# Optimization experiments

Measured on AMD Instinct MI355X. Metric: run time of the kernel, lower is better.

The kernel has to match this reference:

```python
import jax, jax.numpy as jnp
import numpy as np

WS = 32          # window_size; N = WS*WS tokens
NH = 8           # num_heads
HD = 64          # head_dim
DIM = 512        # model dim (= NH*HD)
B = 16
N = WS * WS


def _rel_index() -> np.ndarray:
    """Relative position index, identical to the torch __init__ construction."""
    coords = np.stack(np.meshgrid(np.arange(WS), np.arange(WS), indexing='ij'))
    coords = coords.reshape(2, -1)                       # [2, N]
    rel = coords[:, :, None] - coords[:, None, :]        # [2, N, N]
    rel = rel.transpose(1, 2, 0).copy()                  # [N, N, 2]
    rel[..., 0] += WS - 1
    rel[..., 1] += WS - 1
    rel[..., 0] *= 2 * WS - 1
    return rel.sum(-1).astype(np.int32)                  # [N, N], values in [0, (2WS-1)^2)


def setup_inputs() -> dict:
    key = jax.random.key(0)
    ks = jax.random.split(key, 5)
    s = DIM ** -0.5
    return {
        "x": jax.random.normal(ks[0], (B, N, DIM), jnp.float32),
        "qkv_w": jax.random.normal(ks[1], (3 * NH * HD, DIM), jnp.float32) * s,
        "qkv_b": jnp.zeros((3 * NH * HD,), jnp.float32),
        "proj_w": jax.random.normal(ks[2], (DIM, NH * HD), jnp.float32) * s,
        "proj_b": jnp.zeros((DIM,), jnp.float32),
        "bias_table": jax.random.normal(ks[3], ((2 * WS - 1) ** 2, NH), jnp.float32) * 0.02,
        "rel_index": jnp.asarray(_rel_index()),
    }


def reference(x, qkv_w, qkv_b, proj_w, proj_b, bias_table, rel_index):
    Bb, Nn, C = x.shape
    qkv = (x @ qkv_w.T + qkv_b).reshape(Bb, Nn, 3, NH, HD)
    q, k, v = jnp.moveaxis(qkv, 2, 0)                    # each [B, N, NH, HD]
    q = q * (HD ** -0.5)
    attn = jnp.einsum('bnhd,bmhd->bhnm', q, k)           # [B, NH, N, N]
    bias = bias_table[rel_index]                         # gather -> [N, N, NH]
    attn = attn + jnp.transpose(bias, (2, 0, 1))[None]
    attn = jax.nn.softmax(attn, axis=-1)                 # dropout p=0 (eval)
    out = jnp.einsum('bhnm,bmhd->bnhd', attn, v).reshape(Bb, Nn, NH * HD)
    out = out @ proj_w.T + proj_b                        # [B, N, DIM]
    return jnp.transpose(out, (0, 2, 1)).reshape(Bb, DIM, WS, WS)
```

## Files before the change

kernel.cpp:

```cpp
#include <hip/hip_runtime.h>
#include <hip/hip_bf16.h>


typedef __attribute__((ext_vector_type(4))) float  f32x4;
typedef __attribute__((ext_vector_type(8))) short  s16x8;
typedef __attribute__((ext_vector_type(4))) short  s16x4;

#define LOG2E 1.44269504f

__device__ __forceinline__ short f2bf(float f) {
    union { float f; unsigned u; } v; v.f = f;
    unsigned r = v.u + 0x7fffu + ((v.u >> 16) & 1u);
    return (short)(r >> 16);
}
__device__ __forceinline__ float u2f(unsigned u) {
    union { unsigned u; float f; } v; v.u = u; return v.f;
}
__device__ __forceinline__ unsigned cvtpk(float lo, float hi) {
    unsigned r;
    asm("v_cvt_pk_bf16_f32 %0, %1, %2" : "=v"(r) : "v"(lo), "v"(hi));
    return r;
}
__device__ __forceinline__ s16x8 ld_frag(const short* p) {
    s16x4 lo = *(const s16x4*)p;
    s16x4 hi = *(const s16x4*)(p + 4);
    s16x8 v;
    v[0]=lo[0]; v[1]=lo[1]; v[2]=lo[2]; v[3]=lo[3];
    v[4]=hi[0]; v[5]=hi[1]; v[6]=hi[2]; v[7]=hi[3];
    return v;
}
__device__ __forceinline__ void st8(short* p, s16x8 v) {
    s16x4 lo, hi;
    lo[0]=v[0]; lo[1]=v[1]; lo[2]=v[2]; lo[3]=v[3];
    hi[0]=v[4]; hi[1]=v[5]; hi[2]=v[6]; hi[3]=v[7];
    *(s16x4*)p = lo;
    *(s16x4*)(p + 4) = hi;
}
__device__ __forceinline__ void gl_lds16(const short* g, short* l) {
    __builtin_amdgcn_global_load_lds(
        (const __attribute__((address_space(1))) unsigned int*)g,
        (__attribute__((address_space(3))) unsigned int*)l,
        16, 0, 0);
}

__global__ void cvt_kernel(const float* __restrict__ src, short* __restrict__ dst) {
    int i = blockIdx.x * 256 + threadIdx.x;
    f32x4 v = ((const f32x4*)src)[i];
    s16x4 o;
    o[0]=f2bf(v[0]); o[1]=f2bf(v[1]); o[2]=f2bf(v[2]); o[3]=f2bf(v[3]);
    ((s16x4*)dst)[i] = o;
}

__global__ void bias_expand(const float* __restrict__ table, const int* __restrict__ ridx,
                            short* __restrict__ out) {
    int i = blockIdx.x * 256 + threadIdx.x;
    int n = i >> 10, m = i & 1023;
    int idx = ridx[i];
    const float* t = table + idx * 8;
    int pos = ((n*8 + (m >> 7))*4 + ((m >> 2) & 3))*32 + ((m >> 4) & 7)*4 + (m & 3);
    #pragma unroll
    for (int h = 0; h < 8; h++)
        out[h * 1048576 + pos] = f2bf(t[h] * LOG2E);
}

__global__ __launch_bounds__(256) void qkv_gemm(
    const short* __restrict__ Xb, const short* __restrict__ W,
    const float* __restrict__ bias,
    short* __restrict__ qb, short* __restrict__ kb, short* __restrict__ vtb)
{
    __shared__ __align__(16) short smem[8192];
    short* As = smem;
    short* Bs = smem + 4096;
    const int tid = threadIdx.x;
    const int lane = tid & 63, w = tid >> 6;
    const int quad = lane >> 4, l16 = lane & 15;
    const int m0 = blockIdx.y * 128, n0 = blockIdx.x * 128;
    const int wm = (w >> 1) * 64, wn = (w & 1) * 64;
    f32x4 acc[4][4] = {};

    const int ri = lane >> 2;
    const int u  = lane & 3;

    for (int k0 = 0; k0 < 512; k0 += 32) {
        __syncthreads();
        #pragma unroll
        for (int q = 0; q < 2; q++) {
            int rb = w*32 + q*16;
            int r  = rb + ri;
            int cu = u ^ ((r >> 1) & 3);
            gl_lds16(Xb + (m0 + r)*512 + k0 + cu*8, As + rb*32);
            gl_lds16(W  + (n0 + r)*512 + k0 + cu*8, Bs + rb*32);
        }
        __syncthreads();
        s16x8 af[4], bfr[4];
        #pragma unroll
        for (int i = 0; i < 4; i++) {
            int row = wm + i*16 + l16;
            af[i] = *(const s16x8*)(As + row*32 + (quad ^ ((row >> 1) & 3))*8);
        }
        #pragma unroll
        for (int j = 0; j < 4; j++) {
            int row = wn + j*16 + l16;
            bfr[j] = *(const s16x8*)(Bs + row*32 + (quad ^ ((row >> 1) & 3))*8);
        }
        #pragma unroll
        for (int i = 0; i < 4; i++)
            #pragma unroll
            for (int j = 0; j < 4; j++)
                acc[i][j] = __builtin_amdgcn_mfma_f32_16x16x32_bf16(af[i], bfr[j], acc[i][j], 0, 0, 0);
    }

    #pragma unroll
    for (int j = 0; j < 4; j++) {
        int col = n0 + wn + j*16 + l16;
        int which = col >> 9, rem = col & 511, h = rem >> 6, d = rem & 63;
        float bv = bias[col];
        #pragma unroll
        for (int i = 0; i < 4; i++) {
            int row = m0 + wm + i*16 + quad*4;
            int bi = row >> 10, n = row & 1023;
            if (which == 2) {
                float v0 = acc[i][j][0] + bv, v1 = acc[i][j][1] + bv;
                float v2 = acc[i][j][2] + bv, v3 = acc[i][j][3] + bv;
                uint2 pk; pk.x = cvtpk(v0, v1); pk.y = cvtpk(v2, v3);
                *(uint2*)&vtb[((bi*8 + h)*64 + d)*1024 + n] = pk;
            } else {
                #pragma unroll
                for (int r = 0; r < 4; r++) {
                    float v = acc[i][j][r] + bv;
                    if (which == 0)
                        qb[((bi*8 + h)*1024 + n + r)*64 + d] = f2bf(v * (0.125f * LOG2E));
                    else
                        kb[((bi*8 + h)*1024 + n + r)*64 + d] = f2bf(v);
                }
            }
        }
    }
}

__global__ __launch_bounds__(512, 4) void attn_kernel(
    const short* __restrict__ qbuf, const short* __restrict__ kbuf,
    const short* __restrict__ vtbuf, const short* __restrict__ bxp,
    short* __restrict__ ao)
{
    __shared__ __align__(16) short smem[25344];
    short* R1 = smem;
    short* Vs = smem + 16896;

    const int bh = blockIdx.y;
    const int b = bh >> 3, h = bh & 7;
    const int q0 = blockIdx.x * 128;
    const int tid = threadIdx.x, lane = tid & 63, w = tid >> 6;
    const int quad = lane >> 4, l16 = lane & 15;

    const short* qg = qbuf + (bh*1024 + q0) * 64;
    const short* kg = kbuf + bh * 65536;
    const short* vg = vtbuf + bh * 65536;

    {
        int r = tid >> 3, c = (tid & 7) * 8;
        #pragma unroll
        for (int p = 0; p < 2; p++)
            st8(&R1[(r + p*64)*68 + c], *(const s16x8*)(qg + (r + p*64)*64 + c));
    }
    __syncthreads();
    s16x8 aq[2];
    aq[0] = ld_frag(&R1[(w*16 + l16)*68 + quad*8]);
    aq[1] = ld_frag(&R1[(w*16 + l16)*68 + 32 + quad*8]);

    float mrow = -1e30f, lrow = 0.f;
    f32x4 oacc[4] = {};
    short* Pw = R1 + w * 2112;
    const short* bbase = bxp + h*1048576 + ((q0 + w*16 + l16)*8)*128 + quad*32;

    for (int it = 0; it < 8; it++) {
        const int k0 = it * 128;
        __syncthreads();

        uint4 bw[4];
        {
            const uint4* bp = (const uint4*)(bbase + it*128);
            #pragma unroll
            for (int j = 0; j < 4; j++) bw[j] = bp[j];
        }

        {
            int r = tid >> 3, c = (tid & 7) * 8;
            #pragma unroll
            for (int p = 0; p < 2; p++)
                st8(&R1[(r + p*64)*68 + c], *(const s16x8*)(kg + (k0 + r + p*64)*64 + c));
        }
        {
            int r = tid >> 4, c = (tid & 15) * 8;
            #pragma unroll
            for (int p = 0; p < 2; p++)
                st8(&Vs[(r + p*32)*132 + c], *(const s16x8*)(vg + (r + p*32)*1024 + k0 + c));
        }
        __syncthreads();

        f32x4 s[8];
        __builtin_amdgcn_s_setprio(1);
        #pragma unroll
        for (int nf = 0; nf < 8; nf++) {
            unsigned ua = (nf & 1) ? bw[nf >> 1].z : bw[nf >> 1].x;
            unsigned ub = (nf & 1) ? bw[nf >> 1].w : bw[nf >> 1].y;
            s[nf][0] = u2f(ua << 16); s[nf][1] = u2f(ua & 0xffff0000u);
            s[nf][2] = u2f(ub << 16); s[nf][3] = u2f(ub & 0xffff0000u);
            s16x8 bk0 = ld_frag(&R1[(nf*16 + l16)*68 + quad*8]);
            s16x8 bk1 = ld_frag(&R1[(nf*16 + l16)*68 + 32 + quad*8]);
            s[nf] = __builtin_amdgcn_mfma_f32_16x16x32_bf16(bk0, aq[0], s[nf], 0, 0, 0);
            s[nf] = __builtin_amdgcn_mfma_f32_16x16x32_bf16(bk1, aq[1], s[nf], 0, 0, 0);
        }
        __builtin_amdgcn_s_setprio(0);

        float mx = s[0][0];
        #pragma unroll
        for (int nf = 0; nf < 8; nf++) {
            float a = fmaxf(s[nf][0], s[nf][1]), c = fmaxf(s[nf][2], s[nf][3]);
            mx = fmaxf(mx, fmaxf(a, c));
        }
        if (!__all(mx - mrow <= 8.0f)) {
            float mr = fmaxf(mx, __shfl_xor(mx, 16));
            mr = fmaxf(mr, __shfl_xor(mr, 32));
            float mnew = fmaxf(mrow, mr);
            float alpha = __builtin_exp2f(mrow - mnew);
            mrow = mnew;
            lrow *= alpha;
            float a_r[4];
            #pragma unroll
            for (int r = 0; r < 4; r++) a_r[r] = __shfl(alpha, quad*4 + r);
            #pragma unroll
            for (int df = 0; df < 4; df++)
                #pragma unroll
                for (int r = 0; r < 4; r++)
                    oacc[df][r] *= a_r[r];
        }
        float rs = 0.f;
        #pragma unroll
        for (int nf = 0; nf < 8; nf++)
            #pragma unroll
            for (int r = 0; r < 4; r++) {
                float p = __builtin_exp2f(s[nf][r] - mrow);
                s[nf][r] = p;
                rs += p;
            }
        lrow += rs;

        __syncthreads();

        #pragma unroll
        for (int nf = 0; nf < 8; nf++) {
            uint2 pk;
            pk.x = cvtpk(s[nf][0], s[nf][1]);
            pk.y = cvtpk(s[nf][2], s[nf][3]);
            *(uint2*)&Pw[l16*132 + nf*16 + quad*4] = pk;
        }
        asm volatile("s_waitcnt lgkmcnt(0)" ::: "memory");

        __builtin_amdgcn_s_setprio(1);
        #pragma unroll
        for (int ks = 0; ks < 4; ks++) {
            s16x8 ap = ld_frag(&Pw[l16*132 + ks*32 + quad*8]);
            #pragma unroll
            for (int df = 0; df < 4; df++) {
                s16x8 bv = ld_frag(&Vs[(df*16 + l16)*132 + ks*32 + quad*8]);
                oacc[df] = __builtin_amdgcn_mfma_f32_16x16x32_bf16(ap, bv, oacc[df], 0, 0, 0);
            }
        }
        __builtin_amdgcn_s_setprio(0);
    }

    lrow += __shfl_xor(lrow, 16);
    lrow += __shfl_xor(lrow, 32);
    float inv_r[4];
    #pragma unroll
    for (int r = 0; r < 4; r++) inv_r[r] = 1.0f / __shfl(lrow, quad*4 + r);
    #pragma unroll
    for (int r = 0; r < 4; r++) {
        int n = q0 + w*16 + quad*4 + r;
        #pragma unroll
        for (int df = 0; df < 4; df++)
            ao[(b*1024 + n)*512 + h*64 + df*16 + l16] = f2bf(oacc[df][r] * inv_r[r]);
    }
}

__global__ __launch_bounds__(256) void proj_gemm(
    const short* __restrict__ A, const short* __restrict__ W,
    const float* __restrict__ bias, float* __restrict__ out)
{
    __shared__ __align__(16) short smemp[8448];
    short* As = smemp;
    short* Bs = smemp + 4096;
    const int tid = threadIdx.x;
    const int lane = tid & 63, w = tid >> 6;
    const int quad = lane >> 4, l16 = lane & 15;
    const int m0 = blockIdx.y * 128, n0 = blockIdx.x * 128;
    const int wm = (w >> 1) * 64, wn = (w & 1) * 64;
    f32x4 acc[4][4] = {};

    const int ri = lane >> 2;
    const int u  = lane & 3;

    for (int k0 = 0; k0 < 512; k0 += 32) {
        __syncthreads();
        #pragma unroll
        for (int q = 0; q < 2; q++) {
            int rb = w*32 + q*16;
            int r  = rb + ri;
            int cu = u ^ ((r >> 1) & 3);
            gl_lds16(A + (m0 + r)*512 + k0 + cu*8, As + rb*32);
            gl_lds16(W + (n0 + r)*512 + k0 + cu*8, Bs + rb*32);
        }
        __syncthreads();
        s16x8 af[4], bfr[4];
        #pragma unroll
        for (int i = 0; i < 4; i++) {
            int row = wm + i*16 + l16;
            af[i] = *(const s16x8*)(As + row*32 + (quad ^ ((row >> 1) & 3))*8);
        }
        #pragma unroll
        for (int j = 0; j < 4; j++) {
            int row = wn + j*16 + l16;
            bfr[j] = *(const s16x8*)(Bs + row*32 + (quad ^ ((row >> 1) & 3))*8);
        }
        #pragma unroll
        for (int i = 0; i < 4; i++)
            #pragma unroll
            for (int j = 0; j < 4; j++)
                acc[i][j] = __builtin_amdgcn_mfma_f32_16x16x32_bf16(af[i], bfr[j], acc[i][j], 0, 0, 0);
    }

    const int bi = m0 >> 10, nbase = m0 & 1023;
    float* Ts = (float*)smemp;
    #pragma unroll
    for (int ci = 0; ci < 4; ci++) {
        __syncthreads();
        if ((w & 1) == (ci >> 1)) {
            #pragma unroll
            for (int jj = 0; jj < 2; jj++) {
                int j = (ci & 1) * 2 + jj;
                int c = n0 + wn + j*16 + l16;
                float bv = bias[c];
                int cl = jj*16 + l16;
                #pragma unroll
                for (int i = 0; i < 4; i++) {
                    f32x4 v = acc[i][j];
                    v[0] += bv; v[1] += bv; v[2] += bv; v[3] += bv;
                    *(f32x4*)&Ts[cl*132 + wm + i*16 + quad*4] = v;
                }
            }
        }
        __syncthreads();
        #pragma unroll
        for (int p = 0; p < 4; p++) {
            int row = (tid >> 5) + p*8, col = (tid & 31)*4;
            f32x4 v = *(const f32x4*)&Ts[row*132 + col];
            *(f32x4*)&out[(bi*512 + n0 + ci*32 + row)*1024 + nbase + col] = v;
        }
    }
}

extern "C" void kernel_launch(void* const* d_in, const int* in_sizes, int n_in,
                              void* d_out, int out_size, void* d_ws, size_t ws_size,
                              hipStream_t stream) {
    const float* x      = (const float*)d_in[0];
    const float* qkv_w  = (const float*)d_in[1];
    const float* qkv_b  = (const float*)d_in[2];
    const float* proj_w = (const float*)d_in[3];
    const float* proj_b = (const float*)d_in[4];
    const float* btab   = (const float*)d_in[5];
    const int*   ridx   = (const int*)d_in[6];
    float* out = (float*)d_out;

    short* ws    = (short*)d_ws;
    short* wqkv  = ws;
    short* wproj = wqkv + 1536*512;
    short* qb    = wproj + 512*512;
    short* kb    = qb  + 16*8*1024*64;
    short* vtb   = kb  + 16*8*1024*64;
    short* bx    = vtb + 16*8*1024*64;
    short* ao    = bx  + 8*1024*1024;
    short* xb    = ao;

    cvt_kernel<<<8192, 256, 0, stream>>>(x, xb);
    cvt_kernel<<<768, 256, 0, stream>>>(qkv_w, wqkv);
    cvt_kernel<<<256, 256, 0, stream>>>(proj_w, wproj);
    bias_expand<<<4096, 256, 0, stream>>>(btab, ridx, bx);
    qkv_gemm<<<dim3(12, 128), 256, 0, stream>>>(xb, wqkv, qkv_b, qb, kb, vtb);
    attn_kernel<<<dim3(8, 128), 512, 0, stream>>>(qb, kb, vtb, bx, ao);
    proj_gemm<<<dim3(4, 128), 256, 0, stream>>>(ao, wproj, proj_b, out);
}
```

Measured before the change: 249.1 us.

## Prefetch next K/V tile into registers and widen LDS accesses to 128-bit

The attention kernel now loads the next K and V tiles from global memory into registers while the current tile is being processed, then stores them to LDS at the top of the next iteration. This hides global load latency behind the MFMA and softmax work. LDS row strides change from 68/132 to 72/136 so that 16-byte vector loads and stores stay aligned, which replaces the paired 8-byte accesses. __syncthreads is replaced by an explicit lgkmcnt wait plus s_barrier. In exchange it uses more registers, which may reduce occupancy, and the new padding may change LDS bank conflicts.

```diff
diff --git a/kernel.cpp b/kernel.cpp
--- a/kernel.cpp
+++ b/kernel.cpp
@@ -20,27 +20,16 @@
     unsigned r;
     asm("v_cvt_pk_bf16_f32 %0, %1, %2" : "=v"(r) : "v"(lo), "v"(hi));
     return r;
-}
-__device__ __forceinline__ s16x8 ld_frag(const short* p) {
-    s16x4 lo = *(const s16x4*)p;
-    s16x4 hi = *(const s16x4*)(p + 4);
-    s16x8 v;
-    v[0]=lo[0]; v[1]=lo[1]; v[2]=lo[2]; v[3]=lo[3];
-    v[4]=hi[0]; v[5]=hi[1]; v[6]=hi[2]; v[7]=hi[3];
-    return v;
-}
-__device__ __forceinline__ void st8(short* p, s16x8 v) {
-    s16x4 lo, hi;
-    lo[0]=v[0]; lo[1]=v[1]; lo[2]=v[2]; lo[3]=v[3];
-    hi[0]=v[4]; hi[1]=v[5]; hi[2]=v[6]; hi[3]=v[7];
-    *(s16x4*)p = lo;
-    *(s16x4*)(p + 4) = hi;
 }
 __device__ __forceinline__ void gl_lds16(const short* g, short* l) {
     __builtin_amdgcn_global_load_lds(
         (const __attribute__((address_space(1))) unsigned int*)g,
         (__attribute__((address_space(3))) unsigned int*)l,
         16, 0, 0);
+}
+__device__ __forceinline__ void barrier_lgkm() {
+    asm volatile("s_waitcnt lgkmcnt(0)" ::: "memory");
+    __builtin_amdgcn_s_barrier();
 }
 
 __global__ void cvt_kernel(const float* __restrict__ src, short* __restrict__ dst) {
@@ -143,9 +132,9 @@
     const short* __restrict__ vtbuf, const short* __restrict__ bxp,
     short* __restrict__ ao)
 {
-    __shared__ __align__(16) short smem[25344];
+    __shared__ __align__(16) short smem[26112];
     short* R1 = smem;
-    short* Vs = smem + 16896;
+    short* Vs = smem + 17408;
 
     const int bh = blockIdx.y;
     const int b = bh >> 3, h = bh & 7;
@@ -157,46 +146,51 @@
     const short* kg = kbuf + bh * 65536;
     const short* vg = vtbuf + bh * 65536;
 
+    const int kr = tid >> 3, ku = tid & 7;
+    const int vr = tid >> 4, vu = tid & 15;
+
     {
-        int r = tid >> 3, c = (tid & 7) * 8;
-        #pragma unroll
-        for (int p = 0; p < 2; p++)
-            st8(&R1[(r + p*64)*68 + c], *(const s16x8*)(qg + (r + p*64)*64 + c));
-    }
-    __syncthreads();
-    s16x8 aq[2];
-    aq[0] = ld_frag(&R1[(w*16 + l16)*68 + quad*8]);
-    aq[1] = ld_frag(&R1[(w*16 + l16)*68 + 32 + quad*8]);
+        s16x8 qa = *(const s16x8*)(qg + kr*64 + ku*8);
+        s16x8 qb2 = *(const s16x8*)(qg + (kr+64)*64 + ku*8);
+        *(s16x8*)&R1[kr*72 + ku*8] = qa;
+        *(s16x8*)&R1[(kr+64)*72 + ku*8] = qb2;
+    }
+    barrier_lgkm();
+    s16x8 aq0 = *(const s16x8*)&R1[(w*16 + l16)*72 + quad*8];
+    s16x8 aq1 = *(const s16x8*)&R1[(w*16 + l16)*72 + 32 + quad*8];
+
+    s16x8 kv0 = *(const s16x8*)(kg + kr*64 + ku*8);
+    s16x8 kv1 = *(const s16x8*)(kg + (kr+64)*64 + ku*8);
+    s16x8 vv0 = *(const s16x8*)(vg + vr*1024 + vu*8);
+    s16x8 vv1 = *(const s16x8*)(vg + (vr+32)*1024 + vu*8);
 
     float mrow = -1e30f, lrow = 0.f;
     f32x4 oacc[4] = {};
-    short* Pw = R1 + w * 2112;
+    short* Pw = R1 + w * 2176;
     const short* bbase = bxp + h*1048576 + ((q0 + w*16 + l16)*8)*128 + quad*32;
 
     for (int it = 0; it < 8; it++) {
-        const int k0 = it * 128;
-        __syncthreads();
+        barrier_lgkm();
 
         uint4 bw[4];
         {
             const uint4* bp = (const uint4*)(bbase + it*128);
-            #pragma unroll
-            for (int j = 0; j < 4; j++) bw[j] = bp[j];
-        }
-
-        {
-            int r = tid >> 3, c = (tid & 7) * 8;
-            #pragma unroll
-            for (int p = 0; p < 2; p++)
-                st8(&R1[(r + p*64)*68 + c], *(const s16x8*)(kg + (k0 + r + p*64)*64 + c));
-        }
-        {
-            int r = tid >> 4, c = (tid & 15) * 8;
-            #pragma unroll
-            for (int p = 0; p < 2; p++)
-                st8(&Vs[(r + p*32)*132 + c], *(const s16x8*)(vg + (r + p*32)*1024 + k0 + c));
-        }
-        __syncthreads();
+            bw[0]=bp[0]; bw[1]=bp[1]; bw[2]=bp[2]; bw[3]=bp[3];
+        }
+
+        *(s16x8*)&R1[kr*72 + ku*8]        = kv0;
+        *(s16x8*)&R1[(kr+64)*72 + ku*8]   = kv1;
+        *(s16x8*)&Vs[vr*136 + vu*8]       = vv0;
+        *(s16x8*)&Vs[(vr+32)*136 + vu*8]  = vv1;
+
+        if (it < 7) {
+            const short* kg2 = kg + (it+1)*8192;
+            kv0 = *(const s16x8*)(kg2 + kr*64 + ku*8);
+            kv1 = *(const s16x8*)(kg2 + (kr+64)*64 + ku*8);
+            vv0 = *(const s16x8*)(vg + vr*1024 + (it+1)*128 + vu*8);
+            vv1 = *(const s16x8*)(vg + (vr+32)*1024 + (it+1)*128 + vu*8);
+        }
+        barrier_lgkm();
 
         f32x4 s[8];
         __builtin_amdgcn_s_setprio(1);
@@ -206,10 +200,10 @@
             unsigned ub = (nf & 1) ? bw[nf >> 1].w : bw[nf >> 1].y;
             s[nf][0] = u2f(ua << 16); s[nf][1] = u2f(ua & 0xffff0000u);
             s[nf][2] = u2f(ub << 16); s[nf][3] = u2f(ub & 0xffff0000u);
-            s16x8 bk0 = ld_frag(&R1[(nf*16 + l16)*68 + quad*8]);
-            s16x8 bk1 = ld_frag(&R1[(nf*16 + l16)*68 + 32 + quad*8]);
-            s[nf] = __builtin_amdgcn_mfma_f32_16x16x32_bf16(bk0, aq[0], s[nf], 0, 0, 0);
-            s[nf] = __builtin_amdgcn_mfma_f32_16x16x32_bf16(bk1, aq[1], s[nf], 0, 0, 0);
+            s16x8 bk0 = *(const s16x8*)&R1[(nf*16 + l16)*72 + quad*8];
+            s16x8 bk1 = *(const s16x8*)&R1[(nf*16 + l16)*72 + 32 + quad*8];
+            s[nf] = __builtin_amdgcn_mfma_f32_16x16x32_bf16(bk0, aq0, s[nf], 0, 0, 0);
+            s[nf] = __builtin_amdgcn_mfma_f32_16x16x32_bf16(bk1, aq1, s[nf], 0, 0, 0);
         }
         __builtin_amdgcn_s_setprio(0);
 
@@ -246,24 +240,24 @@
             }
         lrow += rs;
 
-        __syncthreads();
+        barrier_lgkm();
 
         #pragma unroll
         for (int nf = 0; nf < 8; nf++) {
             uint2 pk;
             pk.x = cvtpk(s[nf][0], s[nf][1]);
             pk.y = cvtpk(s[nf][2], s[nf][3]);
-            *(uint2*)&Pw[l16*132 + nf*16 + quad*4] = pk;
+            *(uint2*)&Pw[l16*136 + nf*16 + quad*4] = pk;
         }
         asm volatile("s_waitcnt lgkmcnt(0)" ::: "memory");
 
         __builtin_amdgcn_s_setprio(1);
         #pragma unroll
         for (int ks = 0; ks < 4; ks++) {
-            s16x8 ap = ld_frag(&Pw[l16*132 + ks*32 + quad*8]);
+            s16x8 ap = *(const s16x8*)&Pw[l16*136 + ks*32 + quad*8];
             #pragma unroll
             for (int df = 0; df < 4; df++) {
-                s16x8 bv = ld_frag(&Vs[(df*16 + l16)*132 + ks*32 + quad*8]);
+                s16x8 bv = *(const s16x8*)&Vs[(df*16 + l16)*136 + ks*32 + quad*8];
                 oacc[df] = __builtin_amdgcn_mfma_f32_16x16x32_bf16(ap, bv, oacc[df], 0, 0, 0);
             }
         }
```

After: 252.9 us. No clear change (+1.5%).
